# Performance work log

Hardware: AMD Instinct MI355X
Metric: run time of the kernel (lower is better)

Reference implementation:

```python
import jax, jax.numpy as jnp
import numpy as np

CLIP_VAL = 2.5
NUM_BITS = 8
LN_EPS = 1e-12


def _fake_quant_sym(x, clip_val=CLIP_VAL, num_bits=NUM_BITS):
    """Symmetric layerwise fake quantization with straight-through estimator.

    clamp -> per-tensor scale from max|x| -> round -> dequant. The STE trick
    (x + stop_grad(q - x)) makes the forward value equal to the quantized
    value while the gradient passes through the clamp only.
    """
    qmax = float(2 ** (num_bits - 1) - 1)
    xc = jnp.clip(x, -clip_val, clip_val)
    s = qmax / jnp.maximum(jnp.max(jnp.abs(xc)), 1e-8)
    q = jnp.round(xc * s) / s
    return xc + jax.lax.stop_gradient(q - xc)


def setup_inputs() -> dict:
    key = jax.random.key(0)
    ks = jax.random.split(key, 4)
    B, S, H = 8, 4096, 1024
    return {
        "hidden_states": jax.random.normal(ks[0], (B, S, H), dtype=jnp.float32),
        "input_tensor": jax.random.normal(ks[1], (B, S, H), dtype=jnp.float32),
        "weight": jax.random.normal(ks[2], (H, H), dtype=jnp.float32) * 0.02,
        "bias": jax.random.normal(ks[3], (H,), dtype=jnp.float32) * 0.02,
        "ln_gamma": jnp.ones((H,), dtype=jnp.float32),
        "ln_beta": jnp.zeros((H,), dtype=jnp.float32),
    }


def reference(hidden_states, input_tensor, weight, bias, ln_gamma, ln_beta):
    # QuantizeLinear: fake-quant activations and weight, then GEMM + bias.
    hq = _fake_quant_sym(hidden_states)
    wq = _fake_quant_sym(weight)
    h = jnp.einsum("bsh,oh->bso", hq, wq) + bias  # [B, S, H]
    # Dropout is identity in eval mode. Residual + LayerNorm over last dim.
    y = h + input_tensor
    mu = jnp.mean(y, axis=-1, keepdims=True)
    var = jnp.mean(jnp.square(y - mu), axis=-1, keepdims=True)
    y_norm = (y - mu) * jax.lax.rsqrt(var + LN_EPS)
    return y_norm * ln_gamma + ln_beta
```

## Files before the change

kernel.cpp:

```cpp
#include <hip/hip_runtime.h>
#include <hip/hip_bf16.h>
#include <stdint.h>

#define H_DIM 1024
#define QMAX 127.0f
#define CLIP 2.5f

typedef __attribute__((ext_vector_type(4))) float f32x4;
typedef __attribute__((ext_vector_type(4))) int i32x4;
typedef __attribute__((ext_vector_type(8))) short bf16x8;
typedef __attribute__((ext_vector_type(8))) unsigned short u16x8;
typedef __attribute__((address_space(3))) void lds_void;
typedef const __attribute__((address_space(1))) void gmem_void;

__global__ __launch_bounds__(256) void absmax_clip_kernel(
    const float* __restrict__ x, long n, float* __restrict__ out) {
  float m = 0.f;
  const long stride = (long)gridDim.x * blockDim.x * 4;
  for (long i = ((long)blockIdx.x * blockDim.x + threadIdx.x) * 4; i < n; i += stride) {
    const float4 v = *reinterpret_cast<const float4*>(x + i);
    m = fmaxf(m, fmaxf(fmaxf(fabsf(v.x), fabsf(v.y)), fmaxf(fabsf(v.z), fabsf(v.w))));
  }
  m = fminf(m, CLIP);
#pragma unroll
  for (int off = 32; off > 0; off >>= 1) m = fmaxf(m, __shfl_down(m, off));
  __shared__ float red[4];
  const int lane = threadIdx.x & 63, w = threadIdx.x >> 6;
  if (lane == 0) red[w] = m;
  __syncthreads();
  if (threadIdx.x == 0) {
    const float mm = fmaxf(fmaxf(red[0], red[1]), fmaxf(red[2], red[3]));
    atomicMax(reinterpret_cast<unsigned int*>(out), __float_as_uint(mm));
  }
}

__device__ __forceinline__ unsigned short quant_bf16(float x, float s) {
  const float q = rintf(fminf(fmaxf(x, -CLIP), CLIP) * s);
  return (unsigned short)(__float_as_uint(q) >> 16);
}

__device__ __forceinline__ int quant_i8(float x, float s) {
  return (int)rintf(fminf(fmaxf(x, -CLIP), CLIP) * s);
}

__device__ __forceinline__ unsigned short f2bf_rne(float f) {
  const unsigned u = __float_as_uint(f);
  return (unsigned short)((u + 0x7FFFu + ((u >> 16) & 1u)) >> 16);
}

__device__ __forceinline__ float bf2f(unsigned short u) {
  return __uint_as_float((unsigned)u << 16);
}

__global__ __launch_bounds__(256) void quant_kernel(
    const float* __restrict__ x, unsigned short* __restrict__ q,
    const float* __restrict__ amax_p, long n) {
  const float s = QMAX / fmaxf(amax_p[0], 1e-8f);
  const long stride = (long)gridDim.x * blockDim.x * 4;
  for (long i = ((long)blockIdx.x * blockDim.x + threadIdx.x) * 4; i < n; i += stride) {
    const float4 v = *reinterpret_cast<const float4*>(x + i);
    ushort4 o;
    o.x = quant_bf16(v.x, s);
    o.y = quant_bf16(v.y, s);
    o.z = quant_bf16(v.z, s);
    o.w = quant_bf16(v.w, s);
    *reinterpret_cast<ushort4*>(q + i) = o;
  }
}

__global__ __launch_bounds__(256) void quant8_kernel(
    const float* __restrict__ x, signed char* __restrict__ q,
    const float* __restrict__ amax_p, long n) {
  const float s = QMAX / fmaxf(amax_p[0], 1e-8f);
  const long stride = (long)gridDim.x * blockDim.x * 8;
  for (long i = ((long)blockIdx.x * blockDim.x + threadIdx.x) * 8; i < n; i += stride) {
    const float4 v0 = *reinterpret_cast<const float4*>(x + i);
    const float4 v1 = *reinterpret_cast<const float4*>(x + i + 4);
    unsigned r0 = ((unsigned)(unsigned char)(signed char)quant_i8(v0.x, s)) |
                  ((unsigned)(unsigned char)(signed char)quant_i8(v0.y, s) << 8) |
                  ((unsigned)(unsigned char)(signed char)quant_i8(v0.z, s) << 16) |
                  ((unsigned)(unsigned char)(signed char)quant_i8(v0.w, s) << 24);
    unsigned r1 = ((unsigned)(unsigned char)(signed char)quant_i8(v1.x, s)) |
                  ((unsigned)(unsigned char)(signed char)quant_i8(v1.y, s) << 8) |
                  ((unsigned)(unsigned char)(signed char)quant_i8(v1.z, s) << 16) |
                  ((unsigned)(unsigned char)(signed char)quant_i8(v1.w, s) << 24);
    uint2 o; o.x = r0; o.y = r1;
    *reinterpret_cast<uint2*>(q + i) = o;
  }
}

#define BMs 128
#define BNs 128
#define BKs8 64
#define NIT8 (H_DIM / BKs8)

__global__ __launch_bounds__(256) void gemm_s8_kernel(
    const signed char* __restrict__ Aq8,
    const signed char* __restrict__ Wq8,
    const float* __restrict__ bias,
    const float* __restrict__ scales,
    unsigned short* __restrict__ gbf, int M) {
  __shared__ __attribute__((aligned(16))) char SM8[49152];
  char* As = SM8;
  char* Bs = SM8 + 24576;

  const int nwg = (M / BMs) * 8;
  const int orig = blockIdx.x;
  const int cpx = nwg >> 3;
  const int wg = ((nwg & 7) == 0) ? ((orig & 7) * cpx + (orig >> 3)) : orig;
  const int bn = wg & 7, bm = wg >> 3;
  const int m0 = bm * BMs, n0 = bn * BNs;

  const int t = threadIdx.x;
  const int lane = t & 63, wid = t >> 6;
  const int wr = wid >> 1, wc = wid & 1;
  const int lrow = lane & 15, lgrp = lane >> 4;

  const float amax_h = fmaxf(scales[0], 1e-8f);
  const float amax_w = fmaxf(scales[1], 1e-8f);
  const float inv_s = (amax_h * amax_w) / (QMAX * QMAX);

  const int c0 = t, c1 = t + 256;
  const int r0 = c0 >> 2, r1 = c1 >> 2;
  const unsigned g0 = (unsigned)r0 * H_DIM + (unsigned)((((c0 & 3) ^ ((r0 >> 1) & 3))) * 16);
  const unsigned g1 = (unsigned)r1 * H_DIM + (unsigned)((((c1 & 3) ^ ((r1 >> 1) & 3))) * 16);
  const signed char* Ag = Aq8 + (size_t)m0 * H_DIM;
  const signed char* Bg = Wq8 + (size_t)n0 * H_DIM;

#define STAGE_T8(BUF, KQ)                                                      \
  { __builtin_amdgcn_global_load_lds((gmem_void*)(Ag + g0 + (KQ)),             \
        (lds_void*)(As + (BUF)*8192 + c0 * 16), 16, 0, 0);                     \
    __builtin_amdgcn_global_load_lds((gmem_void*)(Ag + g1 + (KQ)),             \
        (lds_void*)(As + (BUF)*8192 + c1 * 16), 16, 0, 0);                     \
    __builtin_amdgcn_global_load_lds((gmem_void*)(Bg + g0 + (KQ)),             \
        (lds_void*)(Bs + (BUF)*8192 + c0 * 16), 16, 0, 0);                     \
    __builtin_amdgcn_global_load_lds((gmem_void*)(Bg + g1 + (KQ)),             \
        (lds_void*)(Bs + (BUF)*8192 + c1 * 16), 16, 0, 0); }

  int offA[4], offB[4];
#pragma unroll
  for (int i = 0; i < 4; ++i) {
    const int r = wr * 64 + i * 16 + lrow;
    offA[i] = r * 64 + ((lgrp ^ ((r >> 1) & 3)) * 16);
  }
#pragma unroll
  for (int j = 0; j < 4; ++j) {
    const int r = wc * 64 + j * 16 + lrow;
    offB[j] = r * 64 + ((lgrp ^ ((r >> 1) & 3)) * 16);
  }

  i32x4 acc[4][4];
#pragma unroll
  for (int i = 0; i < 4; i++)
#pragma unroll
    for (int j = 0; j < 4; j++)
#pragma unroll
      for (int r = 0; r < 4; r++) acc[i][j][r] = 0;

  STAGE_T8(0, 0)
  STAGE_T8(1, BKs8)

  for (int it = 0; it < NIT8; ++it) {
    const int cb = it % 3;
    if (it + 1 < NIT8) {
      asm volatile("s_waitcnt vmcnt(4)" ::: "memory");
    } else {
      asm volatile("s_waitcnt vmcnt(0)" ::: "memory");
    }
    __builtin_amdgcn_s_barrier();

    i32x4 af[4], bfr[4];
#pragma unroll
    for (int i = 0; i < 4; ++i)
      af[i] = *reinterpret_cast<const i32x4*>(As + cb * 8192 + offA[i]);
#pragma unroll
    for (int j = 0; j < 4; ++j)
      bfr[j] = *reinterpret_cast<const i32x4*>(Bs + cb * 8192 + offB[j]);
    __builtin_amdgcn_s_setprio(1);
#pragma unroll
    for (int i = 0; i < 4; ++i)
#pragma unroll
      for (int j = 0; j < 4; ++j)
        acc[i][j] = __builtin_amdgcn_mfma_i32_16x16x64_i8(af[i], bfr[j], acc[i][j], 0, 0, 0);
    __builtin_amdgcn_s_setprio(0);

    if (it + 2 < NIT8) {
      STAGE_T8((it + 2) % 3, (unsigned)((it + 2) * BKs8))
    }
  }
#undef STAGE_T8
  __syncthreads();

  unsigned short* SMu = reinterpret_cast<unsigned short*>(SM8);
#pragma unroll
  for (int j = 0; j < 4; ++j) {
    const int cl = wc * 64 + j * 16 + lrow;
    const float bv = bias[n0 + cl];
#pragma unroll
    for (int i = 0; i < 4; ++i) {
      const int rl0 = wr * 64 + i * 16 + lgrp * 4;
#pragma unroll
      for (int r = 0; r < 4; ++r)
        SMu[(rl0 + r) * 136 + cl] = f2bf_rne((float)acc[i][j][r] * inv_s + bv);
    }
  }
  __syncthreads();
  {
    const int e_row = t >> 1, e_half = t & 1;
    unsigned short* dst = gbf + (size_t)(m0 + e_row) * H_DIM + n0 + e_half * 64;
    const unsigned short* src = SMu + e_row * 136 + e_half * 64;
#pragma unroll
    for (int c = 0; c < 8; ++c)
      *reinterpret_cast<u16x8*>(dst + c * 8) =
          *reinterpret_cast<const u16x8*>(src + c * 8);
  }
}

__global__ __launch_bounds__(256) void ln_resid_kernel(
    const unsigned short* __restrict__ gbf, const float* __restrict__ resid,
    const float* __restrict__ gamma, const float* __restrict__ beta,
    float* __restrict__ out) {
  const int rl = threadIdx.x >> 7;
  const int c0 = (threadIdx.x & 127) * 8;
  const size_t base = ((size_t)blockIdx.x * 2 + rl) * H_DIM + c0;

  const u16x8 g = *reinterpret_cast<const u16x8*>(gbf + base);
  const float4 rA = *reinterpret_cast<const float4*>(resid + base);
  const float4 rB = *reinterpret_cast<const float4*>(resid + base + 4);
  float v[8];
  v[0] = bf2f(g[0]) + rA.x; v[1] = bf2f(g[1]) + rA.y;
  v[2] = bf2f(g[2]) + rA.z; v[3] = bf2f(g[3]) + rA.w;
  v[4] = bf2f(g[4]) + rB.x; v[5] = bf2f(g[5]) + rB.y;
  v[6] = bf2f(g[6]) + rB.z; v[7] = bf2f(g[7]) + rB.w;

  float s = 0.f, ss = 0.f;
#pragma unroll
  for (int k = 0; k < 8; ++k) { s += v[k]; ss += v[k] * v[k]; }
#pragma unroll
  for (int off = 32; off > 0; off >>= 1) {
    s += __shfl_down(s, off);
    ss += __shfl_down(ss, off);
  }
  __shared__ float red[4][2];
  const int lane = threadIdx.x & 63, w = threadIdx.x >> 6;
  if (lane == 0) { red[w][0] = s; red[w][1] = ss; }
  __syncthreads();
  const int wp = rl * 2;
  const float stot = red[wp][0] + red[wp + 1][0];
  const float sstot = red[wp][1] + red[wp + 1][1];
  const float mu = stot * (1.0f / H_DIM);
  const float var = fmaxf(sstot * (1.0f / H_DIM) - mu * mu, 0.f);
  const float rs = rsqrtf(var + 1e-12f);

  const float4 gA = *reinterpret_cast<const float4*>(gamma + c0);
  const float4 gB = *reinterpret_cast<const float4*>(gamma + c0 + 4);
  const float4 bA = *reinterpret_cast<const float4*>(beta + c0);
  const float4 bB = *reinterpret_cast<const float4*>(beta + c0 + 4);
  float4 oA, oB;
  oA.x = (v[0] - mu) * rs * gA.x + bA.x;
  oA.y = (v[1] - mu) * rs * gA.y + bA.y;
  oA.z = (v[2] - mu) * rs * gA.z + bA.z;
  oA.w = (v[3] - mu) * rs * gA.w + bA.w;
  oB.x = (v[4] - mu) * rs * gB.x + bB.x;
  oB.y = (v[5] - mu) * rs * gB.y + bB.y;
  oB.z = (v[6] - mu) * rs * gB.z + bB.z;
  oB.w = (v[7] - mu) * rs * gB.w + bB.w;
  *reinterpret_cast<float4*>(out + base) = oA;
  *reinterpret_cast<float4*>(out + base + 4) = oB;
}

#define BMv 128
#define BNv 128
#define BKv 32

__global__ __launch_bounds__(256) void gemm_fa_kernel(
    const float* __restrict__ hidden, const unsigned short* __restrict__ Wq,
    const float* __restrict__ bias, const float* __restrict__ resid,
    const float* __restrict__ scales, unsigned short* __restrict__ ybf, int M) {
  __shared__ __attribute__((aligned(16))) unsigned short SM[17408];
  unsigned short* As = SM;
  unsigned short* Bs = SM + 8192;
  const int nwg = (M / BMv) * 8;
  const int orig = blockIdx.x;
  const int cpx = nwg >> 3;
  const int wg = ((nwg & 7) == 0) ? ((orig & 7) * cpx + (orig >> 3)) : orig;
  const int bn = wg & 7, bm = wg >> 3;
  const int m0 = bm * BMv, n0 = bn * BNv;
  const int t = threadIdx.x;
  const int lane = t & 63, wid = t >> 6;
  const int wr = wid >> 1, wc = wid & 1;
  const int lrow = lane & 15, lgrp = lane >> 4;
  const float amax_h = fmaxf(scales[0], 1e-8f);
  const float amax_w = fmaxf(scales[1], 1e-8f);
  const float sh = QMAX / amax_h;
  const float inv_s = (amax_h * amax_w) / (QMAX * QMAX);
  const int a_row = t >> 1, a_half = t & 1;
  const float* Ag = hidden + (size_t)(m0 + a_row) * H_DIM + a_half * 16;
  const int a_swz = (a_row >> 1) & 3;
  const int aw0 = a_row * 32 + (((a_half * 2 + 0) ^ a_swz) * 8);
  const int aw1 = a_row * 32 + (((a_half * 2 + 1) ^ a_swz) * 8);
  const int bc0 = t, bc1 = t + 256;
  const int br0 = bc0 >> 2, br1 = bc1 >> 2;
  const unsigned bg0 = (unsigned)br0 * H_DIM + (unsigned)((((bc0 & 3) ^ ((br0 >> 1) & 3))) * 8);
  const unsigned bg1 = (unsigned)br1 * H_DIM + (unsigned)((((bc1 & 3) ^ ((br1 >> 1) & 3))) * 8);
  const unsigned short* Bg = Wq + (size_t)n0 * H_DIM;
  int offA[4], offB[4];
#pragma unroll
  for (int i = 0; i < 4; ++i) {
    const int r = wr * 64 + i * 16 + lrow;
    offA[i] = r * 32 + ((lgrp ^ ((r >> 1) & 3)) * 8);
  }
#pragma unroll
  for (int j = 0; j < 4; ++j) {
    const int r = wc * 64 + j * 16 + lrow;
    offB[j] = r * 32 + ((lgrp ^ ((r >> 1) & 3)) * 8);
  }
  f32x4 acc[4][4];
#pragma unroll
  for (int i = 0; i < 4; i++)
#pragma unroll
    for (int j = 0; j < 4; j++)
#pragma unroll
      for (int r = 0; r < 4; r++) acc[i][j][r] = 0.f;
#define QUANT_PACK(dst0, dst1, v0, v1, v2, v3)                                 \
  {                                                                            \
    u16x8 p0, p1;                                                              \
    p0[0] = quant_bf16((v0).x, sh); p0[1] = quant_bf16((v0).y, sh);            \
    p0[2] = quant_bf16((v0).z, sh); p0[3] = quant_bf16((v0).w, sh);            \
    p0[4] = quant_bf16((v1).x, sh); p0[5] = quant_bf16((v1).y, sh);            \
    p0[6] = quant_bf16((v1).z, sh); p0[7] = quant_bf16((v1).w, sh);            \
    p1[0] = quant_bf16((v2).x, sh); p1[1] = quant_bf16((v2).y, sh);            \
    p1[2] = quant_bf16((v2).z, sh); p1[3] = quant_bf16((v2).w, sh);            \
    p1[4] = quant_bf16((v3).x, sh); p1[5] = quant_bf16((v3).y, sh);            \
    p1[6] = quant_bf16((v3).z, sh); p1[7] = quant_bf16((v3).w, sh);            \
    *reinterpret_cast<u16x8*>(dst0) = p0;                                      \
    *reinterpret_cast<u16x8*>(dst1) = p1;                                      \
  }
  {
    const float4 v0 = *reinterpret_cast<const float4*>(Ag + 0);
    const float4 v1 = *reinterpret_cast<const float4*>(Ag + 4);
    const float4 v2 = *reinterpret_cast<const float4*>(Ag + 8);
    const float4 v3 = *reinterpret_cast<const float4*>(Ag + 12);
    __builtin_amdgcn_global_load_lds((gmem_void*)(Bg + bg0), (lds_void*)(Bs + bc0 * 8), 16, 0, 0);
    __builtin_amdgcn_global_load_lds((gmem_void*)(Bg + bg1), (lds_void*)(Bs + bc1 * 8), 16, 0, 0);
    QUANT_PACK(As + aw0, As + aw1, v0, v1, v2, v3)
    __syncthreads();
  }
  for (int it = 0; it < H_DIM / BKv; ++it) {
    const int cur = it & 1, nxt = cur ^ 1;
    const bool more = (it + 1) < (H_DIM / BKv);
    float4 v0, v1, v2, v3;
    if (more) {
      const float* Agn = Ag + (it + 1) * BKv;
      v0 = *reinterpret_cast<const float4*>(Agn + 0);
      v1 = *reinterpret_cast<const float4*>(Agn + 4);
      v2 = *reinterpret_cast<const float4*>(Agn + 8);
      v3 = *reinterpret_cast<const float4*>(Agn + 12);
      const unsigned kq = (unsigned)((it + 1) * BKv);
      __builtin_amdgcn_global_load_lds((gmem_void*)(Bg + bg0 + kq),
                                       (lds_void*)(Bs + nxt * 4096 + bc0 * 8), 16, 0, 0);
      __builtin_amdgcn_global_load_lds((gmem_void*)(Bg + bg1 + kq),
                                       (lds_void*)(Bs + nxt * 4096 + bc1 * 8), 16, 0, 0);
    }
    bf16x8 af[4], bfr[4];
#pragma unroll
    for (int i = 0; i < 4; ++i)
      af[i] = *reinterpret_cast<const bf16x8*>(As + cur * 4096 + offA[i]);
#pragma unroll
    for (int j = 0; j < 4; ++j)
      bfr[j] = *reinterpret_cast<const bf16x8*>(Bs + cur * 4096 + offB[j]);
    __builtin_amdgcn_s_setprio(1);
#pragma unroll
    for (int i = 0; i < 4; ++i)
#pragma unroll
      for (int j = 0; j < 4; ++j)
        acc[i][j] = __builtin_amdgcn_mfma_f32_16x16x32_bf16(af[i], bfr[j], acc[i][j], 0, 0, 0);
    __builtin_amdgcn_s_setprio(0);
    if (more) {
      QUANT_PACK(As + nxt * 4096 + aw0, As + nxt * 4096 + aw1, v0, v1, v2, v3)
    }
    __syncthreads();
  }
#pragma unroll
  for (int j = 0; j < 4; ++j) {
    const int cl = wc * 64 + j * 16 + lrow;
    const float bv = bias[n0 + cl];
#pragma unroll
    for (int i = 0; i < 4; ++i) {
      const int rl0 = wr * 64 + i * 16 + lgrp * 4;
#pragma unroll
      for (int r = 0; r < 4; ++r) {
        const float y = acc[i][j][r] * inv_s + bv +
                        resid[(size_t)(m0 + rl0 + r) * H_DIM + n0 + cl];
        SM[(rl0 + r) * 136 + cl] = f2bf_rne(y);
      }
    }
  }
  __syncthreads();
  {
    const int e_row = t >> 1, e_half = t & 1;
    unsigned short* dst = ybf + (size_t)(m0 + e_row) * H_DIM + n0 + e_half * 64;
    const unsigned short* src = SM + e_row * 136 + e_half * 64;
#pragma unroll
    for (int c = 0; c < 8; ++c)
      *reinterpret_cast<u16x8*>(dst + c * 8) =
          *reinterpret_cast<const u16x8*>(src + c * 8);
  }
#undef QUANT_PACK
}

__global__ __launch_bounds__(256) void ln_bf16_kernel(
    const unsigned short* __restrict__ ybf, const float* __restrict__ gamma,
    const float* __restrict__ beta, float* __restrict__ out) {
  const size_t base = (size_t)blockIdx.x * H_DIM + threadIdx.x * 4;
  const ushort4 u = *reinterpret_cast<const ushort4*>(ybf + base);
  float4 v;
  v.x = bf2f(u.x); v.y = bf2f(u.y); v.z = bf2f(u.z); v.w = bf2f(u.w);
  float s = v.x + v.y + v.z + v.w;
  float ss = v.x * v.x + v.y * v.y + v.z * v.z + v.w * v.w;
#pragma unroll
  for (int off = 32; off > 0; off >>= 1) {
    s += __shfl_down(s, off);
    ss += __shfl_down(ss, off);
  }
  __shared__ float red[8];
  const int lane = threadIdx.x & 63, w = threadIdx.x >> 6;
  if (lane == 0) { red[w] = s; red[4 + w] = ss; }
  __syncthreads();
  const float stot = red[0] + red[1] + red[2] + red[3];
  const float sstot = red[4] + red[5] + red[6] + red[7];
  const float mu = stot * (1.0f / H_DIM);
  const float var = fmaxf(sstot * (1.0f / H_DIM) - mu * mu, 0.f);
  const float rs = rsqrtf(var + 1e-12f);
  const float4 g = *reinterpret_cast<const float4*>(gamma + threadIdx.x * 4);
  const float4 b = *reinterpret_cast<const float4*>(beta + threadIdx.x * 4);
  float4 o;
  o.x = (v.x - mu) * rs * g.x + b.x;
  o.y = (v.y - mu) * rs * g.y + b.y;
  o.z = (v.z - mu) * rs * g.z + b.z;
  o.w = (v.w - mu) * rs * g.w + b.w;
  *reinterpret_cast<float4*>(out + base) = o;
}

#define BM 128
#define BN 128
#define BK 32

__global__ __launch_bounds__(256, 2) void gemm_fused_kernel(
    const float* __restrict__ A, const unsigned short* __restrict__ Wq,
    const float* __restrict__ bias, const float* __restrict__ resid,
    const float* __restrict__ scales, float* __restrict__ out, int M) {
  __shared__ unsigned short Asf[BM][40];
  __shared__ unsigned short Bsf[BN][40];
  const int nbm = M / BM;
  const int bm = blockIdx.x % nbm, bn = blockIdx.x / nbm;
  const int m0 = bm * BM, n0 = bn * BN;
  const int t = threadIdx.x;
  const int lane = t & 63, wid = t >> 6;
  const int wr = wid >> 1, wc = wid & 1;
  const int lrow = lane & 15, lgrp = lane >> 4;
  const float amax_h = fmaxf(scales[0], 1e-8f);
  const float amax_w = fmaxf(scales[1], 1e-8f);
  const float sh = QMAX / amax_h;
  const float inv_s = (amax_h * amax_w) / (QMAX * QMAX);
  f32x4 acc[4][4];
#pragma unroll
  for (int i = 0; i < 4; i++)
#pragma unroll
    for (int j = 0; j < 4; j++)
#pragma unroll
      for (int r = 0; r < 4; r++) acc[i][j][r] = 0.f;
  for (int k0 = 0; k0 < H_DIM; k0 += BK) {
#pragma unroll
    for (int j = 0; j < 4; ++j) {
      const int f = j * 256 + t;
      const int r = f >> 3, c4 = f & 7;
      const float4 v = *reinterpret_cast<const float4*>(A + (size_t)(m0 + r) * H_DIM + k0 + c4 * 4);
      ushort4 q;
      q.x = quant_bf16(v.x, sh); q.y = quant_bf16(v.y, sh);
      q.z = quant_bf16(v.z, sh); q.w = quant_bf16(v.w, sh);
      *reinterpret_cast<ushort4*>(&Asf[r][c4 * 4]) = q;
    }
#pragma unroll
    for (int j = 0; j < 2; ++j) {
      const int f = j * 256 + t;
      const int r = f >> 2, cb = f & 3;
      const uint4 v = *reinterpret_cast<const uint4*>(Wq + (size_t)(n0 + r) * H_DIM + k0 + cb * 8);
      *reinterpret_cast<uint4*>(&Bsf[r][cb * 8]) = v;
    }
    __syncthreads();
    bf16x8 af[4], bfr[4];
#pragma unroll
    for (int i = 0; i < 4; i++)
      af[i] = *reinterpret_cast<const bf16x8*>(&Asf[wr * 64 + i * 16 + lrow][lgrp * 8]);
#pragma unroll
    for (int j = 0; j < 4; j++)
      bfr[j] = *reinterpret_cast<const bf16x8*>(&Bsf[wc * 64 + j * 16 + lrow][lgrp * 8]);
#pragma unroll
    for (int i = 0; i < 4; i++)
#pragma unroll
      for (int j = 0; j < 4; j++)
        acc[i][j] = __builtin_amdgcn_mfma_f32_16x16x32_bf16(af[i], bfr[j], acc[i][j], 0, 0, 0);
    __syncthreads();
  }
#pragma unroll
  for (int j = 0; j < 4; j++) {
    const int col = n0 + wc * 64 + j * 16 + lrow;
    const float bv = bias[col];
#pragma unroll
    for (int i = 0; i < 4; i++) {
      const int row0 = m0 + wr * 64 + i * 16 + lgrp * 4;
#pragma unroll
      for (int r = 0; r < 4; r++) {
        const size_t off = (size_t)(row0 + r) * H_DIM + col;
        out[off] = acc[i][j][r] * inv_s + bv + resid[off];
      }
    }
  }
}

__global__ __launch_bounds__(256) void ln_kernel(
    float* __restrict__ y, const float* __restrict__ gamma,
    const float* __restrict__ beta) {
  const size_t base = (size_t)blockIdx.x * H_DIM + threadIdx.x * 4;
  const float4 v = *reinterpret_cast<const float4*>(y + base);
  float s = v.x + v.y + v.z + v.w;
  float ss = v.x * v.x + v.y * v.y + v.z * v.z + v.w * v.w;
#pragma unroll
  for (int off = 32; off > 0; off >>= 1) {
    s += __shfl_down(s, off);
    ss += __shfl_down(ss, off);
  }
  __shared__ float red[8];
  const int lane = threadIdx.x & 63, w = threadIdx.x >> 6;
  if (lane == 0) { red[w] = s; red[4 + w] = ss; }
  __syncthreads();
  const float stot = red[0] + red[1] + red[2] + red[3];
  const float sstot = red[4] + red[5] + red[6] + red[7];
  const float mu = stot * (1.0f / H_DIM);
  const float var = fmaxf(sstot * (1.0f / H_DIM) - mu * mu, 0.f);
  const float rs = rsqrtf(var + 1e-12f);
  const float4 g = *reinterpret_cast<const float4*>(gamma + threadIdx.x * 4);
  const float4 b = *reinterpret_cast<const float4*>(beta + threadIdx.x * 4);
  float4 o;
  o.x = (v.x - mu) * rs * g.x + b.x;
  o.y = (v.y - mu) * rs * g.y + b.y;
  o.z = (v.z - mu) * rs * g.z + b.z;
  o.w = (v.w - mu) * rs * g.w + b.w;
  *reinterpret_cast<float4*>(y + base) = o;
}

extern "C" void kernel_launch(void* const* d_in, const int* in_sizes, int n_in,
                              void* d_out, int out_size, void* d_ws, size_t ws_size,
                              hipStream_t stream) {
  const float* hidden = (const float*)d_in[0];
  const float* resid  = (const float*)d_in[1];
  const float* weight = (const float*)d_in[2];
  const float* bias   = (const float*)d_in[3];
  const float* gamma  = (const float*)d_in[4];
  const float* beta   = (const float*)d_in[5];
  float* out = (float*)d_out;

  const long nh = (long)in_sizes[0];
  const int M = (int)(nh / H_DIM);
  const long nw = (long)H_DIM * H_DIM;

  float* scales = (float*)d_ws;
  char* base = (char*)d_ws + 256;
  signed char* Wq8 = (signed char*)base;
  signed char* Aq8 = (signed char*)(base + nw);
  unsigned short* gbf = (unsigned short*)(base + nw + nh);
  const size_t need1 = 256 + (size_t)nw + (size_t)nh * 3;
  unsigned short* Wq = (unsigned short*)base;
  unsigned short* ybf = (unsigned short*)(base + nw * 2);
  const size_t need2 = 256 + (size_t)nw * 2 + (size_t)nh * 2;

  hipMemsetAsync(d_ws, 0, 8, stream);
  absmax_clip_kernel<<<2048, 256, 0, stream>>>(hidden, nh, scales + 0);
  absmax_clip_kernel<<<256, 256, 0, stream>>>(weight, nw, scales + 1);

  if (ws_size >= need1 && (M % BMs) == 0 && (M % 2) == 0) {
    quant8_kernel<<<512, 256, 0, stream>>>(weight, Wq8, scales + 1, nw);
    quant8_kernel<<<2048, 256, 0, stream>>>(hidden, Aq8, scales + 0, nh);
    gemm_s8_kernel<<<(M / BMs) * (H_DIM / BNs), 256, 0, stream>>>(
        Aq8, Wq8, bias, scales, gbf, M);
    ln_resid_kernel<<<M / 2, 256, 0, stream>>>(gbf, resid, gamma, beta, out);
  } else if (ws_size >= need2 && (M % BMv) == 0) {
    quant_kernel<<<1024, 256, 0, stream>>>(weight, Wq, scales + 1, nw);
    gemm_fa_kernel<<<(M / BMv) * (H_DIM / BNv), 256, 0, stream>>>(
        hidden, Wq, bias, resid, scales, ybf, M);
    ln_bf16_kernel<<<M, 256, 0, stream>>>(ybf, gamma, beta, out);
  } else {
    unsigned short* Wqf = (unsigned short*)base;
    quant_kernel<<<1024, 256, 0, stream>>>(weight, Wqf, scales + 1, nw);
    gemm_fused_kernel<<<(M / BM) * (H_DIM / BN), 256, 0, stream>>>(
        hidden, Wqf, bias, resid, scales, out, M);
    ln_kernel<<<M, 256, 0, stream>>>(out, gamma, beta);
  }
}
```

Before: 198.1 us.

## Fuse absmax and int8 quantization into one cooperative grid-synced kernel

Replaces the two absmax kernels and two int8 quantization kernels with a single cooperative kernel. It computes both absmax values, performs a grid-wide sync, then quantizes hidden and weight to int8. This removes three kernel launches and their serialization gaps, but grid sync has its own cost and the large activation tensor is still read twice. It also removes the unused bf16 fallback GEMM path and checks for cooperative launch support, falling back to the old kernels if it is missing.

Result: slower. 260.8 us (+31.6%).

```diff
diff --git a/kernel.cpp b/kernel.cpp
--- a/kernel.cpp
+++ b/kernel.cpp
@@ -1,6 +1,9 @@
 #include <hip/hip_runtime.h>
 #include <hip/hip_bf16.h>
+#include <hip/hip_cooperative_groups.h>
 #include <stdint.h>
+
+namespace cg = cooperative_groups;
 
 #define H_DIM 1024
 #define QMAX 127.0f
@@ -12,6 +15,87 @@
 typedef __attribute__((ext_vector_type(8))) unsigned short u16x8;
 typedef __attribute__((address_space(3))) void lds_void;
 typedef const __attribute__((address_space(1))) void gmem_void;
+
+__device__ __forceinline__ unsigned short quant_bf16(float x, float s) {
+  const float q = rintf(fminf(fmaxf(x, -CLIP), CLIP) * s);
+  return (unsigned short)(__float_as_uint(q) >> 16);
+}
+
+__device__ __forceinline__ int quant_i8(float x, float s) {
+  return (int)rintf(fminf(fmaxf(x, -CLIP), CLIP) * s);
+}
+
+__device__ __forceinline__ unsigned short f2bf_rne(float f) {
+  const unsigned u = __float_as_uint(f);
+  return (unsigned short)((u + 0x7FFFu + ((u >> 16) & 1u)) >> 16);
+}
+
+__device__ __forceinline__ float bf2f(unsigned short u) {
+  return __uint_as_float((unsigned)u << 16);
+}
+
+__device__ __forceinline__ unsigned pack4_i8(float4 v, float s) {
+  return ((unsigned)(unsigned char)(signed char)quant_i8(v.x, s)) |
+         ((unsigned)(unsigned char)(signed char)quant_i8(v.y, s) << 8) |
+         ((unsigned)(unsigned char)(signed char)quant_i8(v.z, s) << 16) |
+         ((unsigned)(unsigned char)(signed char)quant_i8(v.w, s) << 24);
+}
+
+__global__ __launch_bounds__(256) void coop_quant_kernel(
+    const float* __restrict__ hidden, const float* __restrict__ weight,
+    float* __restrict__ scales, signed char* __restrict__ Aq8,
+    signed char* __restrict__ Wq8, long nh, long nw) {
+  const long tid = (long)blockIdx.x * blockDim.x + threadIdx.x;
+  const long nthr = (long)gridDim.x * blockDim.x;
+
+  float mh = 0.f, mw = 0.f;
+  for (long i = tid * 4; i < nh; i += nthr * 4) {
+    const float4 v = *reinterpret_cast<const float4*>(hidden + i);
+    mh = fmaxf(mh, fmaxf(fmaxf(fabsf(v.x), fabsf(v.y)), fmaxf(fabsf(v.z), fabsf(v.w))));
+  }
+  for (long i = tid * 4; i < nw; i += nthr * 4) {
+    const float4 v = *reinterpret_cast<const float4*>(weight + i);
+    mw = fmaxf(mw, fmaxf(fmaxf(fabsf(v.x), fabsf(v.y)), fmaxf(fabsf(v.z), fabsf(v.w))));
+  }
+  mh = fminf(mh, CLIP);
+  mw = fminf(mw, CLIP);
+#pragma unroll
+  for (int off = 32; off > 0; off >>= 1) {
+    mh = fmaxf(mh, __shfl_down(mh, off));
+    mw = fmaxf(mw, __shfl_down(mw, off));
+  }
+  __shared__ float red[8];
+  const int lane = threadIdx.x & 63, w = threadIdx.x >> 6;
+  if (lane == 0) { red[w] = mh; red[4 + w] = mw; }
+  __syncthreads();
+  if (threadIdx.x == 0) {
+    atomicMax(reinterpret_cast<unsigned int*>(&scales[0]),
+              __float_as_uint(fmaxf(fmaxf(red[0], red[1]), fmaxf(red[2], red[3]))));
+    atomicMax(reinterpret_cast<unsigned int*>(&scales[1]),
+              __float_as_uint(fmaxf(fmaxf(red[4], red[5]), fmaxf(red[6], red[7]))));
+  }
+
+  cg::this_grid().sync();
+
+  const float amax_h = fmaxf(
+      __hip_atomic_load(&scales[0], __ATOMIC_RELAXED, __HIP_MEMORY_SCOPE_AGENT), 1e-8f);
+  const float amax_w = fmaxf(
+      __hip_atomic_load(&scales[1], __ATOMIC_RELAXED, __HIP_MEMORY_SCOPE_AGENT), 1e-8f);
+  const float sh = QMAX / amax_h, sw = QMAX / amax_w;
+
+  for (long i = tid * 8; i < nh; i += nthr * 8) {
+    const float4 v0 = *reinterpret_cast<const float4*>(hidden + i);
+    const float4 v1 = *reinterpret_cast<const float4*>(hidden + i + 4);
+    uint2 o; o.x = pack4_i8(v0, sh); o.y = pack4_i8(v1, sh);
+    *reinterpret_cast<uint2*>(Aq8 + i) = o;
+  }
+  for (long i = tid * 8; i < nw; i += nthr * 8) {
+    const float4 v0 = *reinterpret_cast<const float4*>(weight + i);
+    const float4 v1 = *reinterpret_cast<const float4*>(weight + i + 4);
+    uint2 o; o.x = pack4_i8(v0, sw); o.y = pack4_i8(v1, sw);
+    *reinterpret_cast<uint2*>(Wq8 + i) = o;
+  }
+}
 
 __global__ __launch_bounds__(256) void absmax_clip_kernel(
     const float* __restrict__ x, long n, float* __restrict__ out) {
@@ -32,24 +116,6 @@
     const float mm = fmaxf(fmaxf(red[0], red[1]), fmaxf(red[2], red[3]));
     atomicMax(reinterpret_cast<unsigned int*>(out), __float_as_uint(mm));
   }
-}
-
-__device__ __forceinline__ unsigned short quant_bf16(float x, float s) {
-  const float q = rintf(fminf(fmaxf(x, -CLIP), CLIP) * s);
-  return (unsigned short)(__float_as_uint(q) >> 16);
-}
-
-__device__ __forceinline__ int quant_i8(float x, float s) {
-  return (int)rintf(fminf(fmaxf(x, -CLIP), CLIP) * s);
-}
-
-__device__ __forceinline__ unsigned short f2bf_rne(float f) {
-  const unsigned u = __float_as_uint(f);
-  return (unsigned short)((u + 0x7FFFu + ((u >> 16) & 1u)) >> 16);
-}
-
-__device__ __forceinline__ float bf2f(unsigned short u) {
-  return __uint_as_float((unsigned)u << 16);
 }
 
 __global__ __launch_bounds__(256) void quant_kernel(
@@ -76,15 +142,7 @@
   for (long i = ((long)blockIdx.x * blockDim.x + threadIdx.x) * 8; i < n; i += stride) {
     const float4 v0 = *reinterpret_cast<const float4*>(x + i);
     const float4 v1 = *reinterpret_cast<const float4*>(x + i + 4);
-    unsigned r0 = ((unsigned)(unsigned char)(signed char)quant_i8(v0.x, s)) |
-                  ((unsigned)(unsigned char)(signed char)quant_i8(v0.y, s) << 8) |
-                  ((unsigned)(unsigned char)(signed char)quant_i8(v0.z, s) << 16) |
-                  ((unsigned)(unsigned char)(signed char)quant_i8(v0.w, s) << 24);
-    unsigned r1 = ((unsigned)(unsigned char)(signed char)quant_i8(v1.x, s)) |
-                  ((unsigned)(unsigned char)(signed char)quant_i8(v1.y, s) << 8) |
-                  ((unsigned)(unsigned char)(signed char)quant_i8(v1.z, s) << 16) |
-                  ((unsigned)(unsigned char)(signed char)quant_i8(v1.w, s) << 24);
-    uint2 o; o.x = r0; o.y = r1;
+    uint2 o; o.x = pack4_i8(v0, s); o.y = pack4_i8(v1, s);
     *reinterpret_cast<uint2*>(q + i) = o;
   }
 }
@@ -95,10 +153,8 @@
 #define NIT8 (H_DIM / BKs8)
 
 __global__ __launch_bounds__(256) void gemm_s8_kernel(
-    const signed char* __restrict__ Aq8,
-    const signed char* __restrict__ Wq8,
-    const float* __restrict__ bias,
-    const float* __restrict__ scales,
+    const signed char* __restrict__ Aq8, const signed char* __restrict__ Wq8,
+    const float* __restrict__ bias, const float* __restrict__ scales,
     unsigned short* __restrict__ gbf, int M) {
   __shared__ __attribute__((aligned(16))) char SM8[49152];
   char* As = SM8;
@@ -267,179 +323,6 @@
   oB.w = (v[7] - mu) * rs * gB.w + bB.w;
   *reinterpret_cast<float4*>(out + base) = oA;
   *reinterpret_cast<float4*>(out + base + 4) = oB;
-}
-
-#define BMv 128
-#define BNv 128
-#define BKv 32
-
-__global__ __launch_bounds__(256) void gemm_fa_kernel(
-    const float* __restrict__ hidden, const unsigned short* __restrict__ Wq,
-    const float* __restrict__ bias, const float* __restrict__ resid,
-    const float* __restrict__ scales, unsigned short* __restrict__ ybf, int M) {
-  __shared__ __attribute__((aligned(16))) unsigned short SM[17408];
-  unsigned short* As = SM;
-  unsigned short* Bs = SM + 8192;
-  const int nwg = (M / BMv) * 8;
-  const int orig = blockIdx.x;
-  const int cpx = nwg >> 3;
-  const int wg = ((nwg & 7) == 0) ? ((orig & 7) * cpx + (orig >> 3)) : orig;
-  const int bn = wg & 7, bm = wg >> 3;
-  const int m0 = bm * BMv, n0 = bn * BNv;
-  const int t = threadIdx.x;
-  const int lane = t & 63, wid = t >> 6;
-  const int wr = wid >> 1, wc = wid & 1;
-  const int lrow = lane & 15, lgrp = lane >> 4;
-  const float amax_h = fmaxf(scales[0], 1e-8f);
-  const float amax_w = fmaxf(scales[1], 1e-8f);
-  const float sh = QMAX / amax_h;
-  const float inv_s = (amax_h * amax_w) / (QMAX * QMAX);
-  const int a_row = t >> 1, a_half = t & 1;
-  const float* Ag = hidden + (size_t)(m0 + a_row) * H_DIM + a_half * 16;
-  const int a_swz = (a_row >> 1) & 3;
-  const int aw0 = a_row * 32 + (((a_half * 2 + 0) ^ a_swz) * 8);
-  const int aw1 = a_row * 32 + (((a_half * 2 + 1) ^ a_swz) * 8);
-  const int bc0 = t, bc1 = t + 256;
-  const int br0 = bc0 >> 2, br1 = bc1 >> 2;
-  const unsigned bg0 = (unsigned)br0 * H_DIM + (unsigned)((((bc0 & 3) ^ ((br0 >> 1) & 3))) * 8);
-  const unsigned bg1 = (unsigned)br1 * H_DIM + (unsigned)((((bc1 & 3) ^ ((br1 >> 1) & 3))) * 8);
-  const unsigned short* Bg = Wq + (size_t)n0 * H_DIM;
-  int offA[4], offB[4];
-#pragma unroll
-  for (int i = 0; i < 4; ++i) {
-    const int r = wr * 64 + i * 16 + lrow;
-    offA[i] = r * 32 + ((lgrp ^ ((r >> 1) & 3)) * 8);
-  }
-#pragma unroll
-  for (int j = 0; j < 4; ++j) {
-    const int r = wc * 64 + j * 16 + lrow;
-    offB[j] = r * 32 + ((lgrp ^ ((r >> 1) & 3)) * 8);
-  }
-  f32x4 acc[4][4];
-#pragma unroll
-  for (int i = 0; i < 4; i++)
-#pragma unroll
-    for (int j = 0; j < 4; j++)
-#pragma unroll
-      for (int r = 0; r < 4; r++) acc[i][j][r] = 0.f;
-#define QUANT_PACK(dst0, dst1, v0, v1, v2, v3)                                 \
-  {                                                                            \
-    u16x8 p0, p1;                                                              \
-    p0[0] = quant_bf16((v0).x, sh); p0[1] = quant_bf16((v0).y, sh);            \
-    p0[2] = quant_bf16((v0).z, sh); p0[3] = quant_bf16((v0).w, sh);            \
-    p0[4] = quant_bf16((v1).x, sh); p0[5] = quant_bf16((v1).y, sh);            \
-    p0[6] = quant_bf16((v1).z, sh); p0[7] = quant_bf16((v1).w, sh);            \
-    p1[0] = quant_bf16((v2).x, sh); p1[1] = quant_bf16((v2).y, sh);            \
-    p1[2] = quant_bf16((v2).z, sh); p1[3] = quant_bf16((v2).w, sh);            \
-    p1[4] = quant_bf16((v3).x, sh); p1[5] = quant_bf16((v3).y, sh);            \
-    p1[6] = quant_bf16((v3).z, sh); p1[7] = quant_bf16((v3).w, sh);            \
-    *reinterpret_cast<u16x8*>(dst0) = p0;                                      \
-    *reinterpret_cast<u16x8*>(dst1) = p1;                                      \
-  }
-  {
-    const float4 v0 = *reinterpret_cast<const float4*>(Ag + 0);
-    const float4 v1 = *reinterpret_cast<const float4*>(Ag + 4);
-    const float4 v2 = *reinterpret_cast<const float4*>(Ag + 8);
-    const float4 v3 = *reinterpret_cast<const float4*>(Ag + 12);
-    __builtin_amdgcn_global_load_lds((gmem_void*)(Bg + bg0), (lds_void*)(Bs + bc0 * 8), 16, 0, 0);
-    __builtin_amdgcn_global_load_lds((gmem_void*)(Bg + bg1), (lds_void*)(Bs + bc1 * 8), 16, 0, 0);
-    QUANT_PACK(As + aw0, As + aw1, v0, v1, v2, v3)
-    __syncthreads();
-  }
-  for (int it = 0; it < H_DIM / BKv; ++it) {
-    const int cur = it & 1, nxt = cur ^ 1;
-    const bool more = (it + 1) < (H_DIM / BKv);
-    float4 v0, v1, v2, v3;
-    if (more) {
-      const float* Agn = Ag + (it + 1) * BKv;
-      v0 = *reinterpret_cast<const float4*>(Agn + 0);
-      v1 = *reinterpret_cast<const float4*>(Agn + 4);
-      v2 = *reinterpret_cast<const float4*>(Agn + 8);
-      v3 = *reinterpret_cast<const float4*>(Agn + 12);
-      const unsigned kq = (unsigned)((it + 1) * BKv);
-      __builtin_amdgcn_global_load_lds((gmem_void*)(Bg + bg0 + kq),
-                                       (lds_void*)(Bs + nxt * 4096 + bc0 * 8), 16, 0, 0);
-      __builtin_amdgcn_global_load_lds((gmem_void*)(Bg + bg1 + kq),
-                                       (lds_void*)(Bs + nxt * 4096 + bc1 * 8), 16, 0, 0);
-    }
-    bf16x8 af[4], bfr[4];
-#pragma unroll
-    for (int i = 0; i < 4; ++i)
-      af[i] = *reinterpret_cast<const bf16x8*>(As + cur * 4096 + offA[i]);
-#pragma unroll
-    for (int j = 0; j < 4; ++j)
-      bfr[j] = *reinterpret_cast<const bf16x8*>(Bs + cur * 4096 + offB[j]);
-    __builtin_amdgcn_s_setprio(1);
-#pragma unroll
-    for (int i = 0; i < 4; ++i)
-#pragma unroll
-      for (int j = 0; j < 4; ++j)
-        acc[i][j] = __builtin_amdgcn_mfma_f32_16x16x32_bf16(af[i], bfr[j], acc[i][j], 0, 0, 0);
-    __builtin_amdgcn_s_setprio(0);
-    if (more) {
-      QUANT_PACK(As + nxt * 4096 + aw0, As + nxt * 4096 + aw1, v0, v1, v2, v3)
-    }
-    __syncthreads();
-  }
-#pragma unroll
-  for (int j = 0; j < 4; ++j) {
-    const int cl = wc * 64 + j * 16 + lrow;
-    const float bv = bias[n0 + cl];
-#pragma unroll
-    for (int i = 0; i < 4; ++i) {
-      const int rl0 = wr * 64 + i * 16 + lgrp * 4;
-#pragma unroll
-      for (int r = 0; r < 4; ++r) {
-        const float y = acc[i][j][r] * inv_s + bv +
-                        resid[(size_t)(m0 + rl0 + r) * H_DIM + n0 + cl];
-        SM[(rl0 + r) * 136 + cl] = f2bf_rne(y);
-      }
-    }
-  }
-  __syncthreads();
-  {
-    const int e_row = t >> 1, e_half = t & 1;
-    unsigned short* dst = ybf + (size_t)(m0 + e_row) * H_DIM + n0 + e_half * 64;
-    const unsigned short* src = SM + e_row * 136 + e_half * 64;
-#pragma unroll
-    for (int c = 0; c < 8; ++c)
-      *reinterpret_cast<u16x8*>(dst + c * 8) =
-          *reinterpret_cast<const u16x8*>(src + c * 8);
-  }
-#undef QUANT_PACK
-}
-
-__global__ __launch_bounds__(256) void ln_bf16_kernel(
-    const unsigned short* __restrict__ ybf, const float* __restrict__ gamma,
-    const float* __restrict__ beta, float* __restrict__ out) {
-  const size_t base = (size_t)blockIdx.x * H_DIM + threadIdx.x * 4;
-  const ushort4 u = *reinterpret_cast<const ushort4*>(ybf + base);
-  float4 v;
-  v.x = bf2f(u.x); v.y = bf2f(u.y); v.z = bf2f(u.z); v.w = bf2f(u.w);
-  float s = v.x + v.y + v.z + v.w;
-  float ss = v.x * v.x + v.y * v.y + v.z * v.z + v.w * v.w;
-#pragma unroll
-  for (int off = 32; off > 0; off >>= 1) {
-    s += __shfl_down(s, off);
-    ss += __shfl_down(ss, off);
-  }
-  __shared__ float red[8];
-  const int lane = threadIdx.x & 63, w = threadIdx.x >> 6;
-  if (lane == 0) { red[w] = s; red[4 + w] = ss; }
-  __syncthreads();
-  const float stot = red[0] + red[1] + red[2] + red[3];
-  const float sstot = red[4] + red[5] + red[6] + red[7];
-  const float mu = stot * (1.0f / H_DIM);
-  const float var = fmaxf(sstot * (1.0f / H_DIM) - mu * mu, 0.f);
-  const float rs = rsqrtf(var + 1e-12f);
-  const float4 g = *reinterpret_cast<const float4*>(gamma + threadIdx.x * 4);
-  const float4 b = *reinterpret_cast<const float4*>(beta + threadIdx.x * 4);
-  float4 o;
-  o.x = (v.x - mu) * rs * g.x + b.x;
-  o.y = (v.y - mu) * rs * g.y + b.y;
-  o.z = (v.z - mu) * rs * g.z + b.z;
-  o.w = (v.w - mu) * rs * g.w + b.w;
-  *reinterpret_cast<float4*>(out + base) = o;
 }
 
 #define BM 128
@@ -571,27 +454,38 @@
   signed char* Aq8 = (signed char*)(base + nw);
   unsigned short* gbf = (unsigned short*)(base + nw + nh);
   const size_t need1 = 256 + (size_t)nw + (size_t)nh * 3;
-  unsigned short* Wq = (unsigned short*)base;
-  unsigned short* ybf = (unsigned short*)(base + nw * 2);
-  const size_t need2 = 256 + (size_t)nw * 2 + (size_t)nh * 2;
+  const size_t need3 = 256 + (size_t)nw * 2;
 
   hipMemsetAsync(d_ws, 0, 8, stream);
-  absmax_clip_kernel<<<2048, 256, 0, stream>>>(hidden, nh, scales + 0);
-  absmax_clip_kernel<<<256, 256, 0, stream>>>(weight, nw, scales + 1);
-
-  if (ws_size >= need1 && (M % BMs) == 0 && (M % 2) == 0) {
-    quant8_kernel<<<512, 256, 0, stream>>>(weight, Wq8, scales + 1, nw);
-    quant8_kernel<<<2048, 256, 0, stream>>>(hidden, Aq8, scales + 0, nh);
+
+  if (ws_size >= need1 && (M % BMs) == 0 && (M % 2) == 0 && (nh % 8) == 0) {
+    int dev = 0, coop_ok = 0;
+    hipGetDevice(&dev);
+    hipDeviceGetAttribute(&coop_ok, hipDeviceAttributeCooperativeLaunch, dev);
+    bool used_coop = false;
+    if (coop_ok) {
+      long nh_a = nh, nw_a = nw;
+      const float* h_a = hidden; const float* w_a = weight;
+      float* s_a = scales; signed char* a_a = Aq8; signed char* q_a = Wq8;
+      void* args[] = {(void*)&h_a, (void*)&w_a, (void*)&s_a,
+                      (void*)&a_a, (void*)&q_a, (void*)&nh_a, (void*)&nw_a};
+      hipError_t e = hipLaunchCooperativeKernel(
+          (const void*)coop_quant_kernel, dim3(1024), dim3(256), args, 0, stream);
+      used_coop = (e == hipSuccess);
+    }
+    if (!used_coop) {
+      absmax_clip_kernel<<<2048, 256, 0, stream>>>(hidden, nh, scales + 0);
+      absmax_clip_kernel<<<256, 256, 0, stream>>>(weight, nw, scales + 1);
+      quant8_kernel<<<512, 256, 0, stream>>>(weight, Wq8, scales + 1, nw);
+      quant8_kernel<<<2048, 256, 0, stream>>>(hidden, Aq8, scales + 0, nh);
+    }
     gemm_s8_kernel<<<(M / BMs) * (H_DIM / BNs), 256, 0, stream>>>(
         Aq8, Wq8, bias, scales, gbf, M);
     ln_resid_kernel<<<M / 2, 256, 0, stream>>>(gbf, resid, gamma, beta, out);
-  } else if (ws_size >= need2 && (M % BMv) == 0) {
-    quant_kernel<<<1024, 256, 0, stream>>>(weight, Wq, scales + 1, nw);
-    gemm_fa_kernel<<<(M / BMv) * (H_DIM / BNv), 256, 0, stream>>>(
-        hidden, Wq, bias, resid, scales, ybf, M);
-    ln_bf16_kernel<<<M, 256, 0, stream>>>(ybf, gamma, beta, out);
-  } else {
+  } else if (ws_size >= need3 && (M % BM) == 0) {
     unsigned short* Wqf = (unsigned short*)base;
+    absmax_clip_kernel<<<2048, 256, 0, stream>>>(hidden, nh, scales + 0);
+    absmax_clip_kernel<<<256, 256, 0, stream>>>(weight, nw, scales + 1);
     quant_kernel<<<1024, 256, 0, stream>>>(weight, Wqf, scales + 1, nw);
     gemm_fused_kernel<<<(M / BM) * (H_DIM / BN), 256, 0, stream>>>(
         hidden, Wqf, bias, resid, scales, out, M);
```
